# Optimization experiments

Hardware: AMD Instinct MI355X
Metric: run time of the kernel (lower is better)

## Reference

```python
import jax, jax.numpy as jnp
import numpy as np

EPSILON = 0.01            # params.epsilon (cluster precision regularizer)
GAMMA = 0.005             # params.gamma (outlier/uniform component weight)
FIX_CLUSTER_POS_ITER = 1  # params.fix_cluster_pos_iter


def _sqdist(TVs, X):
    # TVs: (M, 3, N) transformed points, X: (K, 3) cluster means -> (M, N, K)
    return ((TVs ** 2).sum(1)[:, :, None]
            + (X ** 2).sum(1)[None, None, :]
            - 2.0 * jnp.einsum('mdn,kd->mnk', TVs, X))


def setup_inputs() -> dict:
    key = jax.random.key(0)
    kV, kX, kQ = jax.random.split(key, 3)
    M, N, K = 8, 8192, 256
    Vs = jax.random.normal(kV, (M, 3, N), dtype=jnp.float32)      # 3D point clouds
    X0 = jax.random.normal(kX, (K, 3), dtype=jnp.float32)         # init cluster means (sphere init)
    Q0 = 0.1 + 0.2 * jax.random.uniform(kQ, (K,), dtype=jnp.float32)  # init cluster precisions
    return {"Vs": Vs, "X0": X0, "Q0": Q0, "num_iters": 6}


def reference(Vs, X0, Q0, num_iters):
    M, _, N = Vs.shape
    K = X0.shape[0]
    dtype = Vs.dtype

    # mean_init: init_R = I, init_t = -mean(V) per view
    t0 = -Vs.mean(axis=2, keepdims=True)          # (M, 3, 1)
    TVs = Vs + t0
    beta = GAMMA * jnp.mean(Q0) ** 1.5            # get_default_beta(Q, gamma)

    X, Q = X0, Q0
    ds = _sqdist(TVs, X)                          # (M, N, K)
    R = jnp.broadcast_to(jnp.eye(3, dtype=dtype), (M, 3, 3))
    t = t0[:, :, 0]

    for i in range(num_iters):
        if i != num_iters - 1:  # detach everything except backprop_iter = [last]
            X = jax.lax.stop_gradient(X)
            Q = jax.lax.stop_gradient(Q)
            ds = jax.lax.stop_gradient(ds)

        # E-step: soft posteriors with uniform outlier component beta
        ap = jnp.exp(-0.5 * ds * Q) * Q ** 1.5    # (M, N, K); priors = 1, pyz_feature = 1
        a = ap / (ap.sum(axis=-1, keepdims=True) + beta)

        # M-step: weighted sufficient statistics
        L = a.sum(axis=1)                                   # (M, K)
        W = jnp.einsum('mdn,mnk->mdk', Vs, a) * Q           # (M, 3, K)
        mW = W.sum(axis=-1)                                 # (M, 3)
        b = L * Q                                           # (M, K)
        mX = jnp.einsum('mk,kd->md', b, X)                  # (M, 3)
        z = b.sum(axis=-1)                                  # (M,)

        # P = (W @ X)^T - mX mW^T / z  : 3x3 weighted cross-covariance per view
        P = (jnp.einsum('mdk,ke->med', W, X)
             - mX[:, :, None] * mW[:, None, :] / z[:, None, None])

        # batched Procrustes: R = U diag(1,1,det(U V^T)) V^T
        U, _, Vt = jnp.linalg.svd(P)
        det = jnp.linalg.det(jnp.einsum('mij,mjk->mik', U, Vt))
        sgn = jnp.concatenate([jnp.ones((M, 2), dtype), det[:, None]], axis=1)
        R = jnp.einsum('mij,mjk->mik', U * sgn[:, None, :], Vt)   # (M, 3, 3)
        t = (mX - jnp.einsum('mij,mj->mi', R, mW)) / z[:, None]   # (M, 3)
        TVs = jnp.einsum('mij,mjn->min', R, Vs) + t[:, :, None]   # (M, 3, N)

        # shared cluster updates (sum over views)
        den = L.sum(axis=0)                                 # (K,)
        if i > FIX_CLUSTER_POS_ITER:
            X = jnp.einsum('mdn,mnk->kd', TVs, a) / den[:, None]
        ds = _sqdist(TVs, X)
        wn = (a * ds).sum(axis=(0, 1))                      # (K,)
        Q = 3.0 * den / (wn + 3.0 * den * EPSILON)

    return TVs, R, t, X
```

## Files before the change

kernel.cpp:

```cpp
#include <hip/hip_runtime.h>
#include <math.h>

#define Mv 8
#define Nv 8192
#define Kv 256
#define BPM 64
#define NBLK (Mv*BPM)
#define NITER 6
#define EPSILON_C 0.01f
#define GAMMA_C 0.005f

#define WS_R     0
#define WS_T     72
#define WS_X     96
#define WS_Q     864
#define WS_BETA  1120
#define WS_ACC   1124
#define AC_STATS 0
#define AC_L     128
#define AC_W     2176
#define AC_H     8320
#define ACCSZ    10368

__device__ __forceinline__ float wave_red_sum(float x) {
  int v;
  float t;
  v = __builtin_bit_cast(int, x);
  t = __builtin_bit_cast(float, __builtin_amdgcn_update_dpp(0, v, 0x111, 0xf, 0xf, true));
  x += t; v = __builtin_bit_cast(int, x);
  t = __builtin_bit_cast(float, __builtin_amdgcn_update_dpp(0, v, 0x112, 0xf, 0xf, true));
  x += t; v = __builtin_bit_cast(int, x);
  t = __builtin_bit_cast(float, __builtin_amdgcn_update_dpp(0, v, 0x114, 0xf, 0xf, true));
  x += t; v = __builtin_bit_cast(int, x);
  t = __builtin_bit_cast(float, __builtin_amdgcn_update_dpp(0, v, 0x118, 0xf, 0xf, true));
  x += t; v = __builtin_bit_cast(int, x);
  t = __builtin_bit_cast(float, __builtin_amdgcn_update_dpp(0, v, 0x142, 0xa, 0xf, false));
  x += t; v = __builtin_bit_cast(int, x);
  t = __builtin_bit_cast(float, __builtin_amdgcn_update_dpp(0, v, 0x143, 0xc, 0xf, false));
  x += t;
  return __builtin_bit_cast(float, __builtin_amdgcn_readlane(__builtin_bit_cast(int, x), 63));
}

__global__ __launch_bounds__(256) void p0_init(const float* __restrict__ Vs,
                                               const float* __restrict__ X0,
                                               const float* __restrict__ Q0,
                                               float* __restrict__ ws) {
  __shared__ float sred[4];
  int tid = threadIdx.x;
  int b = blockIdx.x;
  int wave = tid >> 6, lane = tid & 63;
  if (b < 24) {
    int m = b / 3, d = b % 3;
    const float* src = Vs + (size_t)(m*3 + d) * Nv;
    float s = 0.f;
    for (int n = tid; n < Nv; n += 256) s += src[n];
    s = wave_red_sum(s);
    if (lane == 0) sred[wave] = s;
    __syncthreads();
    if (tid == 0) {
      float tot = sred[0]+sred[1]+sred[2]+sred[3];
      ws[WS_T + m*3 + d] = -tot / (float)Nv;
    }
    if (d == 0 && tid < 9) {
      ws[WS_R + m*9 + tid] = (tid==0||tid==4||tid==8) ? 1.f : 0.f;
    }
  } else {
    float s = (tid < Kv) ? Q0[tid] : 0.f;
    s = wave_red_sum(s);
    if (lane == 0) sred[wave] = s;
    __syncthreads();
    if (tid == 0) {
      float mq = (sred[0]+sred[1]+sred[2]+sred[3]) / (float)Kv;
      ws[WS_BETA] = GAMMA_C * mq * sqrtf(mq);
    }
    if (tid < Kv) ws[WS_Q + tid] = Q0[tid];
    for (int i = tid; i < Kv*3; i += 256) ws[WS_X + i] = X0[i];
    for (int i = tid; i < ACCSZ; i += 256) ws[WS_ACC + i] = 0.f;
  }
}

#define JROTF(app,aqq,apq,apr,aqr, vp0,vp1,vp2, vq0,vq1,vq2) do {           \
    float tau_ = (aqq - app) * __builtin_amdgcn_rcpf(2.0f*apq);             \
    float tt_ = __builtin_amdgcn_rcpf(fabsf(tau_) +                         \
                   __builtin_amdgcn_sqrtf(fmaf(tau_,tau_,1.0f)));           \
    tt_ = (tau_ < 0.0f) ? -tt_ : tt_;                                       \
    tt_ = (apq == 0.0f) ? 0.0f : tt_;                                       \
    float c_ = __builtin_amdgcn_rsqf(fmaf(tt_,tt_,1.0f)), s_ = tt_*c_;      \
    float papq_ = apq;                                                      \
    app = fmaf(-tt_,papq_,app); aqq = fmaf(tt_,papq_,aqq); apq = 0.0f;      \
    float tp_ = apr, tq_ = aqr;                                             \
    apr = c_*tp_ - s_*tq_; aqr = s_*tp_ + c_*tq_;                           \
    tp_=vp0; tq_=vq0; vp0=c_*tp_-s_*tq_; vq0=s_*tp_+c_*tq_;                 \
    tp_=vp1; tq_=vq1; vp1=c_*tp_-s_*tq_; vq1=s_*tp_+c_*tq_;                 \
    tp_=vp2; tq_=vq2; vp2=c_*tp_-s_*tq_; vq2=s_*tp_+c_*tq_;                 \
  } while(0)

#define CSWAP3F(la,lb, a0,a1,a2, b0,b1,b2) do {                             \
    if (la < lb) { float t_;                                                \
      t_=la; la=lb; lb=t_; t_=a0; a0=b0; b0=t_;                             \
      t_=a1; a1=b1; b1=t_; t_=a2; a2=b2; b2=t_; }                           \
  } while(0)

template<int ITPREV>
__device__ __forceinline__ void small_update(const float* __restrict__ acc,
                                             const float* __restrict__ ws,
                                             int tid,
                                             float (*sX)[3], float* sQ,
                                             float (*sR)[9], float (*sT)[3],
                                             float* sTn) {
  const int k = tid;
  float lk[Mv], w0v[Mv], w1v[Mv], w2v[Mv], hk[Mv];
  #pragma unroll
  for (int mm=0;mm<Mv;mm++) {
    lk[mm]  = acc[AC_L + mm*Kv + k];
    w0v[mm] = acc[AC_W + (mm*3+0)*Kv + k];
    w1v[mm] = acc[AC_W + (mm*3+1)*Kv + k];
    w2v[mm] = acc[AC_W + (mm*3+2)*Kv + k];
    hk[mm]  = acc[AC_H + mm*Kv + k];
  }
  float xp0 = 0.f, xp1 = 0.f, xp2 = 0.f;
  if (ITPREV <= 1) {
    xp0 = ws[WS_X + k*3+0]; xp1 = ws[WS_X + k*3+1]; xp2 = ws[WS_X + k*3+2];
  }

  if (tid < Mv) {
    int mm = tid;
    const float* st = acc + AC_STATS + mm*16;
    float s0=st[0], s1=st[1], s2v=st[2], s3=st[3], s4=st[4], s5=st[5],
          s6=st[6], s7=st[7], s8=st[8], s9=st[9], s10=st[10], s11=st[11],
          s12=st[12], s13=st[13], s14=st[14], s15=st[15];
    float z = s0;
    float mX0 = s1, mX1 = s2v, mX2 = s3;
    float mW0 = s4, mW1 = s5, mW2 = s6;
    float iz = __builtin_amdgcn_rcpf(z);
    float P00 = s7  - mX0*mW0*iz;
    float P01 = s8  - mX0*mW1*iz;
    float P02 = s9  - mX0*mW2*iz;
    float P10 = s10 - mX1*mW0*iz;
    float P11 = s11 - mX1*mW1*iz;
    float P12 = s12 - mX1*mW2*iz;
    float P20 = s13 - mX2*mW0*iz;
    float P21 = s14 - mX2*mW1*iz;
    float P22 = s15 - mX2*mW2*iz;
    float a00 = P00*P00 + P10*P10 + P20*P20;
    float a01 = P00*P01 + P10*P11 + P20*P21;
    float a02 = P00*P02 + P10*P12 + P20*P22;
    float a11 = P01*P01 + P11*P11 + P21*P21;
    float a12 = P01*P02 + P11*P12 + P21*P22;
    float a22 = P02*P02 + P12*P12 + P22*P22;
    float v00=1, v01=0, v02=0, v10=0, v11=1, v12=0, v20=0, v21=0, v22=1;
    #pragma unroll 1
    for (int sweep = 0; sweep < 8; sweep++) {
      JROTF(a00,a11,a01, a02,a12, v00,v10,v20, v01,v11,v21);
      JROTF(a00,a22,a02, a01,a12, v00,v10,v20, v02,v12,v22);
      JROTF(a11,a22,a12, a01,a02, v01,v11,v21, v02,v12,v22);
    }
    float l0 = a00, l1 = a11, l2 = a22;
    CSWAP3F(l0,l1, v00,v10,v20, v01,v11,v21);
    CSWAP3F(l1,l2, v01,v11,v21, v02,v12,v22);
    CSWAP3F(l0,l1, v00,v10,v20, v01,v11,v21);
    float detP = P00*(P11*P22-P12*P21) - P01*(P10*P22-P12*P20)
               + P02*(P10*P21-P11*P20);
    float s2d = (detP < 0.0f) ? -1.0f : 1.0f;
    float tiny = 1e-18f*l0 + 1e-30f;
    float w0i = __builtin_amdgcn_rsqf(fmaxf(l0,tiny));
    float w1i = __builtin_amdgcn_rsqf(fmaxf(l1,tiny));
    float w2i = s2d*__builtin_amdgcn_rsqf(fmaxf(l2,tiny));
    float M00 = w0i*v00*v00 + w1i*v01*v01 + w2i*v02*v02;
    float M01 = w0i*v00*v10 + w1i*v01*v11 + w2i*v02*v12;
    float M02 = w0i*v00*v20 + w1i*v01*v21 + w2i*v02*v22;
    float M11 = w0i*v10*v10 + w1i*v11*v11 + w2i*v12*v12;
    float M12 = w0i*v10*v20 + w1i*v11*v21 + w2i*v12*v22;
    float M22 = w0i*v20*v20 + w1i*v21*v21 + w2i*v22*v22;
    float R00n = P00*M00 + P01*M01 + P02*M02;
    float R01n = P00*M01 + P01*M11 + P02*M12;
    float R02n = P00*M02 + P01*M12 + P02*M22;
    float R10n = P10*M00 + P11*M01 + P12*M02;
    float R11n = P10*M01 + P11*M11 + P12*M12;
    float R12n = P10*M02 + P11*M12 + P12*M22;
    float R20n = P20*M00 + P21*M01 + P22*M02;
    float R21n = P20*M01 + P21*M11 + P22*M12;
    float R22n = P20*M02 + P21*M12 + P22*M22;
    float tm0 = (mX0 - (R00n*mW0 + R01n*mW1 + R02n*mW2))*iz;
    float tm1 = (mX1 - (R10n*mW0 + R11n*mW1 + R12n*mW2))*iz;
    float tm2 = (mX2 - (R20n*mW0 + R21n*mW1 + R22n*mW2))*iz;
    sR[mm][0]=R00n; sR[mm][1]=R01n; sR[mm][2]=R02n;
    sR[mm][3]=R10n; sR[mm][4]=R11n; sR[mm][5]=R12n;
    sR[mm][6]=R20n; sR[mm][7]=R21n; sR[mm][8]=R22n;
    sT[mm][0]=tm0; sT[mm][1]=tm1; sT[mm][2]=tm2;
    sTn[mm] = tm0*tm0 + tm1*tm1 + tm2*tm2;
  }
  __syncthreads();
  {
    float den = 0.f, Xn0=0.f, Xn1=0.f, Xn2=0.f, S2=0.f;
    #pragma unroll
    for (int mm=0;mm<Mv;mm++) {
      float r0 = sR[mm][0]*w0v[mm] + sR[mm][1]*w1v[mm] + sR[mm][2]*w2v[mm];
      float r1 = sR[mm][3]*w0v[mm] + sR[mm][4]*w1v[mm] + sR[mm][5]*w2v[mm];
      float r2 = sR[mm][6]*w0v[mm] + sR[mm][7]*w1v[mm] + sR[mm][8]*w2v[mm];
      float tt0 = sT[mm][0], tt1 = sT[mm][1], tt2 = sT[mm][2];
      den += lk[mm];
      Xn0 += r0 + tt0*lk[mm]; Xn1 += r1 + tt1*lk[mm]; Xn2 += r2 + tt2*lk[mm];
      S2  += hk[mm] + 2.f*(tt0*r0+tt1*r1+tt2*r2) + sTn[mm]*lk[mm];
    }
    float x0, x1, x2;
    if (ITPREV > 1) { float inv = __builtin_amdgcn_rcpf(den);
                      x0=Xn0*inv; x1=Xn1*inv; x2=Xn2*inv; }
    else            { x0=xp0; x1=xp1; x2=xp2; }
    float wn = S2 + (x0*x0+x1*x1+x2*x2)*den - 2.f*(x0*Xn0+x1*Xn1+x2*Xn2);
    float qn = 3.f*den / (wn + 3.f*den*EPSILON_C);
    sX[k][0]=x0; sX[k][1]=x1; sX[k][2]=x2;
    sQ[k] = qn;
  }
}

template<int IT>
__global__ __launch_bounds__(256) void p_iter(const float* __restrict__ Vs,
                                              float* __restrict__ ws) {
  __shared__ float sb[4][5][Kv];
  __shared__ float st4[4][16];
  __shared__ float sX[Kv][3];
  __shared__ float sQ[Kv];
  __shared__ float sR[Mv][9];
  __shared__ float sT[Mv][3];
  __shared__ float sTn[Mv];

  int tid  = threadIdx.x;
  int wave = tid >> 6, lane = tid & 63;
  int bid  = blockIdx.x;
  int m    = bid / BPM;
  int blk  = bid % BPM;
  int wid  = blk*4 + wave;
  const int k = tid;

  float* acc  = ws + WS_ACC + (IT % 3)*ACCSZ;
  float* accz = ws + WS_ACC + ((IT+1) % 3)*ACCSZ;
  float beta = ws[WS_BETA];

  if (IT == 0) {
    if (tid < 72) ((float*)sR)[tid] = ws[WS_R + tid];
    if (tid < 24) ((float*)sT)[tid] = ws[WS_T + tid];
    sX[k][0] = ws[WS_X + 3*k+0];
    sX[k][1] = ws[WS_X + 3*k+1];
    sX[k][2] = ws[WS_X + 3*k+2];
    sQ[k]    = ws[WS_Q + k];
  } else {
    const float* accp = ws + WS_ACC + ((IT+2) % 3)*ACCSZ;
    small_update<(IT > 0) ? (IT-1) : 0>(accp, ws, tid, sX, sQ, sR, sT, sTn);
  }
  __syncthreads();

  { int base = bid*21;
    if (tid < 21 && base + tid < ACCSZ) accz[base + tid] = 0.f; }

  float R00=sR[m][0],R01=sR[m][1],R02=sR[m][2];
  float R10=sR[m][3],R11=sR[m][4],R12=sR[m][5];
  float R20=sR[m][6],R21=sR[m][7],R22=sR[m][8];
  float t0=sT[m][0], t1=sT[m][1], t2=sT[m][2];
  float kXx[4],kXy[4],kXz[4],kA[4],kB[4],kQ[4],kQ32[4];
  #pragma unroll
  for (int j=0;j<4;j++) {
    int kk = lane + 64*j;
    float xx = sX[kk][0], xy = sX[kk][1], xz = sX[kk][2];
    float q  = sQ[kk];
    kXx[j]=xx; kXy[j]=xy; kXz[j]=xz;
    kA[j]  = -0.5f*q;
    kB[j]  = kA[j]*(xx*xx+xy*xy+xz*xz);
    kQ[j]  = q;
    kQ32[j]= q*sqrtf(q);
  }
  float aL[4]={0,0,0,0}, aWx[4]={0,0,0,0}, aWy[4]={0,0,0,0},
        aWz[4]={0,0,0,0}, aH[4]={0,0,0,0};
  const float* V0 = Vs + (size_t)(m*3+0)*Nv;
  const float* V1 = Vs + (size_t)(m*3+1)*Nv;
  const float* V2 = Vs + (size_t)(m*3+2)*Nv;
  for (int n = wid; n < Nv; n += 256) {
    float vx = V0[n], vy = V1[n], vz = V2[n];
    float px = fmaf(R00,vx, fmaf(R01,vy, fmaf(R02,vz, t0)));
    float py = fmaf(R10,vx, fmaf(R11,vy, fmaf(R12,vz, t1)));
    float pz = fmaf(R20,vx, fmaf(R21,vy, fmaf(R22,vz, t2)));
    float tvn = fmaf(px,px, fmaf(py,py, pz*pz));
    float vn  = fmaf(vx,vx, fmaf(vy,vy, vz*vz));
    float ap[4]; float s = 0.f;
    #pragma unroll
    for (int j=0;j<4;j++) {
      float dot = fmaf(px,kXx[j], fmaf(py,kXy[j], pz*kXz[j]));
      float arg = fmaf(kQ[j], dot, fmaf(kA[j], tvn, kB[j]));
      float e = __expf(arg)*kQ32[j];
      ap[j] = e; s += e;
    }
    float S = wave_red_sum(s);
    float inv = __builtin_amdgcn_rcpf(S + beta);
    #pragma unroll
    for (int j=0;j<4;j++) {
      float a = ap[j]*inv;
      aL[j] += a;
      aWx[j] = fmaf(a,vx,aWx[j]);
      aWy[j] = fmaf(a,vy,aWy[j]);
      aWz[j] = fmaf(a,vz,aWz[j]);
      aH[j]  = fmaf(a,vn,aH[j]);
    }
  }
  #pragma unroll
  for (int j=0;j<4;j++) {
    int kk = lane + 64*j;
    sb[wave][0][kk]=aL[j];  sb[wave][1][kk]=aWx[j]; sb[wave][2][kk]=aWy[j];
    sb[wave][3][kk]=aWz[j]; sb[wave][4][kk]=aH[j];
  }
  __syncthreads();
  const int k2 = (tid + 4*blk) & (Kv-1);
  float vL  = sb[0][0][k2]+sb[1][0][k2]+sb[2][0][k2]+sb[3][0][k2];
  float vWx = sb[0][1][k2]+sb[1][1][k2]+sb[2][1][k2]+sb[3][1][k2];
  float vWy = sb[0][2][k2]+sb[1][2][k2]+sb[2][2][k2]+sb[3][2][k2];
  float vWz = sb[0][3][k2]+sb[1][3][k2]+sb[2][3][k2]+sb[3][3][k2];
  float vH  = sb[0][4][k2]+sb[1][4][k2]+sb[2][4][k2]+sb[3][4][k2];
  atomicAdd(&acc[AC_L + m*Kv + k2], vL);
  atomicAdd(&acc[AC_W + (m*3+0)*Kv + k2], vWx);
  atomicAdd(&acc[AC_W + (m*3+1)*Kv + k2], vWy);
  atomicAdd(&acc[AC_W + (m*3+2)*Kv + k2], vWz);
  atomicAdd(&acc[AC_H + m*Kv + k2], vH);
  {
    float q  = sQ[k2];
    float x0 = sX[k2][0], x1 = sX[k2][1], x2 = sX[k2][2];
    float bk = vL*q;
    float sw0 = vWx*q, sw1 = vWy*q, sw2 = vWz*q;
    float pr[16];
    pr[0]=bk;  pr[1]=bk*x0; pr[2]=bk*x1; pr[3]=bk*x2;
    pr[4]=sw0; pr[5]=sw1;   pr[6]=sw2;
    pr[7]=sw0*x0;  pr[8]=sw1*x0;  pr[9]=sw2*x0;
    pr[10]=sw0*x1; pr[11]=sw1*x1; pr[12]=sw2*x1;
    pr[13]=sw0*x2; pr[14]=sw1*x2; pr[15]=sw2*x2;
    float red[16];
    #pragma unroll
    for (int v2=0; v2<16; v2++) red[v2] = wave_red_sum(pr[v2]);
    if (lane == 0) {
      #pragma unroll
      for (int v2=0; v2<16; v2++) st4[wave][v2] = red[v2];
    }
    __syncthreads();
    if (tid < 16)
      atomicAdd(&acc[AC_STATS + m*16 + ((tid + blk) & 15)],
                st4[0][(tid+blk)&15]+st4[1][(tid+blk)&15]+
                st4[2][(tid+blk)&15]+st4[3][(tid+blk)&15]);
  }
}

#define OUT_TOTAL (Mv*3*Nv + 72 + 24 + Kv*3)
__global__ __launch_bounds__(256) void p3_final(const float* __restrict__ Vs,
                                                const float* __restrict__ ws,
                                                float* __restrict__ out) {
  __shared__ float sX[Kv][3];
  __shared__ float sQ[Kv];
  __shared__ float sR[Mv][9];
  __shared__ float sT[Mv][3];
  __shared__ float sTn[Mv];
  int tid = threadIdx.x;
  const float* acc = ws + WS_ACC + ((NITER-1) % 3)*ACCSZ;
  small_update<NITER-1>(acc, ws, tid, sX, sQ, sR, sT, sTn);
  __syncthreads();

  for (int idx = blockIdx.x*256 + tid; idx < OUT_TOTAL; idx += 256*256) {
    if (idx < Mv*3*Nv) {
      int m = idx / (3*Nv);
      int r = idx % (3*Nv);
      int d = r / Nv;
      int n = r % Nv;
      float vx = Vs[(size_t)(m*3+0)*Nv + n];
      float vy = Vs[(size_t)(m*3+1)*Nv + n];
      float vz = Vs[(size_t)(m*3+2)*Nv + n];
      out[idx] = fmaf(sR[m][d*3+0],vx,
                 fmaf(sR[m][d*3+1],vy,
                 fmaf(sR[m][d*3+2],vz, sT[m][d])));
    } else {
      int j = idx - Mv*3*Nv;
      float v;
      if (j < 72)      v = ((float*)sR)[j];
      else if (j < 96) v = ((float*)sT)[j-72];
      else             v = ((float*)sX)[j-96];
      out[idx] = v;
    }
  }
}

extern "C" void kernel_launch(void* const* d_in, const int* in_sizes, int n_in,
                              void* d_out, int out_size, void* d_ws, size_t ws_size,
                              hipStream_t stream) {
  const float* Vs = (const float*)d_in[0];
  const float* X0 = (const float*)d_in[1];
  const float* Q0 = (const float*)d_in[2];
  float* out = (float*)d_out;
  float* ws  = (float*)d_ws;

  p0_init<<<25, 256, 0, stream>>>(Vs, X0, Q0, ws);
  p_iter<0><<<NBLK, 256, 0, stream>>>(Vs, ws);
  p_iter<1><<<NBLK, 256, 0, stream>>>(Vs, ws);
  p_iter<2><<<NBLK, 256, 0, stream>>>(Vs, ws);
  p_iter<3><<<NBLK, 256, 0, stream>>>(Vs, ws);
  p_iter<4><<<NBLK, 256, 0, stream>>>(Vs, ws);
  p_iter<5><<<NBLK, 256, 0, stream>>>(Vs, ws);
  p3_final<<<256, 256, 0, stream>>>(Vs, ws, out);
}
```

Measured before the change: 213.2 us.

## Run per-iteration small update once in last-arriving block instead of every block

Before, every one of the 512 blocks redundantly recomputed the cluster/rotation update (small_update, including the Jacobi SVD) at the start of each iteration. Now a ticket counter picks the last block to finish accumulation, and that block alone computes the 16 per-view statistics from the accumulated per-cluster sums and then the Procrustes and cluster update. It writes R, t, X and Q to global workspace for the next launch to read. This removes redundant per-block work and the per-block stats atomics, at the cost of a serial tail in one block per iteration. The accumulators switch to double buffering, and the final kernel reads from global memory with more blocks.

```diff
diff --git a/kernel.cpp b/kernel.cpp
--- a/kernel.cpp
+++ b/kernel.cpp
@@ -12,15 +12,15 @@
 
 #define WS_R     0
 #define WS_T     72
-#define WS_X     96
-#define WS_Q     864
+#define WS_XC    96
+#define WS_QC    864
 #define WS_BETA  1120
-#define WS_ACC   1124
-#define AC_STATS 0
-#define AC_L     128
-#define AC_W     2176
-#define AC_H     8320
-#define ACCSZ    10368
+#define WS_TKT   1124
+#define WS_ACC   1132
+#define AC_L     0
+#define AC_W     2048
+#define AC_H     8192
+#define ACCSZ    10240
 
 __device__ __forceinline__ float wave_red_sum(float x) {
   int v;
@@ -64,7 +64,7 @@
     if (d == 0 && tid < 9) {
       ws[WS_R + m*9 + tid] = (tid==0||tid==4||tid==8) ? 1.f : 0.f;
     }
-  } else {
+  } else if (b == 24) {
     float s = (tid < Kv) ? Q0[tid] : 0.f;
     s = wave_red_sum(s);
     if (lane == 0) sred[wave] = s;
@@ -73,9 +73,11 @@
       float mq = (sred[0]+sred[1]+sred[2]+sred[3]) / (float)Kv;
       ws[WS_BETA] = GAMMA_C * mq * sqrtf(mq);
     }
-    if (tid < Kv) ws[WS_Q + tid] = Q0[tid];
-    for (int i = tid; i < Kv*3; i += 256) ws[WS_X + i] = X0[i];
-    for (int i = tid; i < ACCSZ; i += 256) ws[WS_ACC + i] = 0.f;
+    if (tid < Kv) ws[WS_QC + tid] = Q0[tid];
+    for (int i = tid; i < Kv*3; i += 256) ws[WS_XC + i] = X0[i];
+  } else {
+    for (int i = tid + (b-25)*256; i < 8 + ACCSZ; i += 256*8)
+      ws[WS_TKT + i] = 0.f;
   }
 }
 
@@ -101,13 +103,110 @@
       t_=a1; a1=b1; b1=t_; t_=a2; a2=b2; b2=t_; }                           \
   } while(0)
 
-template<int ITPREV>
-__device__ __forceinline__ void small_update(const float* __restrict__ acc,
-                                             const float* __restrict__ ws,
-                                             int tid,
-                                             float (*sX)[3], float* sQ,
-                                             float (*sR)[9], float (*sT)[3],
-                                             float* sTn) {
+template<int IT>
+__global__ __launch_bounds__(256) void p_iter(const float* __restrict__ Vs,
+                                              float* __restrict__ ws) {
+  __shared__ float sb[4][5][Kv];
+  __shared__ float st4[4][128];
+  __shared__ float sStats[Mv][16];
+  __shared__ float sR[Mv][9];
+  __shared__ float sT[Mv][3];
+  __shared__ float sTn[Mv];
+  __shared__ int   sLast;
+
+  int tid  = threadIdx.x;
+  int wave = tid >> 6, lane = tid & 63;
+  int bid  = blockIdx.x;
+  int m    = bid / BPM;
+  int blk  = bid % BPM;
+  int wid  = blk*4 + wave;
+
+  float* acc  = ws + WS_ACC + (IT & 1)*ACCSZ;
+  float* accz = ws + WS_ACC + ((IT+1) & 1)*ACCSZ;
+  float beta = ws[WS_BETA];
+
+  if (tid < 20) accz[bid*20 + tid] = 0.f;
+
+  float R00=ws[WS_R+m*9+0], R01=ws[WS_R+m*9+1], R02=ws[WS_R+m*9+2];
+  float R10=ws[WS_R+m*9+3], R11=ws[WS_R+m*9+4], R12=ws[WS_R+m*9+5];
+  float R20=ws[WS_R+m*9+6], R21=ws[WS_R+m*9+7], R22=ws[WS_R+m*9+8];
+  float t0=ws[WS_T+m*3+0], t1=ws[WS_T+m*3+1], t2=ws[WS_T+m*3+2];
+  float kXx[4],kXy[4],kXz[4],kA[4],kB[4],kQ[4],kQ32[4];
+  #pragma unroll
+  for (int j=0;j<4;j++) {
+    int kk = lane + 64*j;
+    float xx = ws[WS_XC+kk*3+0], xy = ws[WS_XC+kk*3+1], xz = ws[WS_XC+kk*3+2];
+    float q  = ws[WS_QC+kk];
+    kXx[j]=xx; kXy[j]=xy; kXz[j]=xz;
+    kA[j]  = -0.5f*q;
+    kB[j]  = kA[j]*(xx*xx+xy*xy+xz*xz);
+    kQ[j]  = q;
+    kQ32[j]= q*sqrtf(q);
+  }
+
+  float aL[4]={0,0,0,0}, aWx[4]={0,0,0,0}, aWy[4]={0,0,0,0},
+        aWz[4]={0,0,0,0}, aH[4]={0,0,0,0};
+  const float* V0 = Vs + (size_t)(m*3+0)*Nv;
+  const float* V1 = Vs + (size_t)(m*3+1)*Nv;
+  const float* V2 = Vs + (size_t)(m*3+2)*Nv;
+  for (int n = wid; n < Nv; n += 256) {
+    float vx = V0[n], vy = V1[n], vz = V2[n];
+    float px = fmaf(R00,vx, fmaf(R01,vy, fmaf(R02,vz, t0)));
+    float py = fmaf(R10,vx, fmaf(R11,vy, fmaf(R12,vz, t1)));
+    float pz = fmaf(R20,vx, fmaf(R21,vy, fmaf(R22,vz, t2)));
+    float tvn = fmaf(px,px, fmaf(py,py, pz*pz));
+    float vn  = fmaf(vx,vx, fmaf(vy,vy, vz*vz));
+    float ap[4]; float s = 0.f;
+    #pragma unroll
+    for (int j=0;j<4;j++) {
+      float dot = fmaf(px,kXx[j], fmaf(py,kXy[j], pz*kXz[j]));
+      float arg = fmaf(kQ[j], dot, fmaf(kA[j], tvn, kB[j]));
+      float e = __expf(arg)*kQ32[j];
+      ap[j] = e; s += e;
+    }
+    float S = wave_red_sum(s);
+    float inv = __builtin_amdgcn_rcpf(S + beta);
+    #pragma unroll
+    for (int j=0;j<4;j++) {
+      float a = ap[j]*inv;
+      aL[j] += a;
+      aWx[j] = fmaf(a,vx,aWx[j]);
+      aWy[j] = fmaf(a,vy,aWy[j]);
+      aWz[j] = fmaf(a,vz,aWz[j]);
+      aH[j]  = fmaf(a,vn,aH[j]);
+    }
+  }
+  #pragma unroll
+  for (int j=0;j<4;j++) {
+    int kk = lane + 64*j;
+    sb[wave][0][kk]=aL[j];  sb[wave][1][kk]=aWx[j]; sb[wave][2][kk]=aWy[j];
+    sb[wave][3][kk]=aWz[j]; sb[wave][4][kk]=aH[j];
+  }
+  __syncthreads();
+  {
+    const int k2 = (tid + 4*blk) & (Kv-1);
+    float vL  = sb[0][0][k2]+sb[1][0][k2]+sb[2][0][k2]+sb[3][0][k2];
+    float vWx = sb[0][1][k2]+sb[1][1][k2]+sb[2][1][k2]+sb[3][1][k2];
+    float vWy = sb[0][2][k2]+sb[1][2][k2]+sb[2][2][k2]+sb[3][2][k2];
+    float vWz = sb[0][3][k2]+sb[1][3][k2]+sb[2][3][k2]+sb[3][3][k2];
+    float vH  = sb[0][4][k2]+sb[1][4][k2]+sb[2][4][k2]+sb[3][4][k2];
+    atomicAdd(&acc[AC_L + m*Kv + k2], vL);
+    atomicAdd(&acc[AC_W + (m*3+0)*Kv + k2], vWx);
+    atomicAdd(&acc[AC_W + (m*3+1)*Kv + k2], vWy);
+    atomicAdd(&acc[AC_W + (m*3+2)*Kv + k2], vWz);
+    atomicAdd(&acc[AC_H + m*Kv + k2], vH);
+  }
+
+  __threadfence();
+  __syncthreads();
+  if (tid == 0) {
+    unsigned old = atomicAdd((unsigned*)(ws + WS_TKT) + IT, 1u);
+    sLast = (old == (unsigned)(NBLK - 1));
+  }
+  __syncthreads();
+  if (!sLast) return;
+  __threadfence();
+
   const int k = tid;
   float lk[Mv], w0v[Mv], w1v[Mv], w2v[Mv], hk[Mv];
   #pragma unroll
@@ -118,17 +217,36 @@
     w2v[mm] = acc[AC_W + (mm*3+2)*Kv + k];
     hk[mm]  = acc[AC_H + mm*Kv + k];
   }
-  float xp0 = 0.f, xp1 = 0.f, xp2 = 0.f;
-  if (ITPREV <= 1) {
-    xp0 = ws[WS_X + k*3+0]; xp1 = ws[WS_X + k*3+1]; xp2 = ws[WS_X + k*3+2];
-  }
+  float qk  = ws[WS_QC + k];
+  float xc0 = ws[WS_XC + k*3+0], xc1 = ws[WS_XC + k*3+1], xc2 = ws[WS_XC + k*3+2];
+
+  #pragma unroll
+  for (int mm=0;mm<Mv;mm++) {
+    float bk  = lk[mm]*qk;
+    float sw0 = w0v[mm]*qk, sw1 = w1v[mm]*qk, sw2 = w2v[mm]*qk;
+    float pr[16];
+    pr[0]=bk;  pr[1]=bk*xc0; pr[2]=bk*xc1; pr[3]=bk*xc2;
+    pr[4]=sw0; pr[5]=sw1;    pr[6]=sw2;
+    pr[7]=sw0*xc0;  pr[8]=sw1*xc0;  pr[9]=sw2*xc0;
+    pr[10]=sw0*xc1; pr[11]=sw1*xc1; pr[12]=sw2*xc1;
+    pr[13]=sw0*xc2; pr[14]=sw1*xc2; pr[15]=sw2*xc2;
+    #pragma unroll
+    for (int v2=0; v2<16; v2++) {
+      float r = wave_red_sum(pr[v2]);
+      if (lane == 0) st4[wave][mm*16+v2] = r;
+    }
+  }
+  __syncthreads();
+  if (tid < 128)
+    sStats[tid>>4][tid&15] = st4[0][tid]+st4[1][tid]+st4[2][tid]+st4[3][tid];
+  __syncthreads();
 
   if (tid < Mv) {
     int mm = tid;
-    const float* st = acc + AC_STATS + mm*16;
-    float s0=st[0], s1=st[1], s2v=st[2], s3=st[3], s4=st[4], s5=st[5],
-          s6=st[6], s7=st[7], s8=st[8], s9=st[9], s10=st[10], s11=st[11],
-          s12=st[12], s13=st[13], s14=st[14], s15=st[15];
+    float s0=sStats[mm][0], s1=sStats[mm][1], s2v=sStats[mm][2], s3=sStats[mm][3],
+          s4=sStats[mm][4], s5=sStats[mm][5], s6=sStats[mm][6], s7=sStats[mm][7],
+          s8=sStats[mm][8], s9=sStats[mm][9], s10=sStats[mm][10], s11=sStats[mm][11],
+          s12=sStats[mm][12], s13=sStats[mm][13], s14=sStats[mm][14], s15=sStats[mm][15];
     float z = s0;
     float mX0 = s1, mX1 = s2v, mX2 = s3;
     float mW0 = s4, mW1 = s5, mW2 = s6;
@@ -204,162 +322,23 @@
       S2  += hk[mm] + 2.f*(tt0*r0+tt1*r1+tt2*r2) + sTn[mm]*lk[mm];
     }
     float x0, x1, x2;
-    if (ITPREV > 1) { float inv = __builtin_amdgcn_rcpf(den);
-                      x0=Xn0*inv; x1=Xn1*inv; x2=Xn2*inv; }
-    else            { x0=xp0; x1=xp1; x2=xp2; }
+    if (IT > 1) { float inv = __builtin_amdgcn_rcpf(den);
+                  x0=Xn0*inv; x1=Xn1*inv; x2=Xn2*inv; }
+    else        { x0=xc0; x1=xc1; x2=xc2; }
     float wn = S2 + (x0*x0+x1*x1+x2*x2)*den - 2.f*(x0*Xn0+x1*Xn1+x2*Xn2);
     float qn = 3.f*den / (wn + 3.f*den*EPSILON_C);
-    sX[k][0]=x0; sX[k][1]=x1; sX[k][2]=x2;
-    sQ[k] = qn;
-  }
-}
-
-template<int IT>
-__global__ __launch_bounds__(256) void p_iter(const float* __restrict__ Vs,
-                                              float* __restrict__ ws) {
-  __shared__ float sb[4][5][Kv];
-  __shared__ float st4[4][16];
-  __shared__ float sX[Kv][3];
-  __shared__ float sQ[Kv];
-  __shared__ float sR[Mv][9];
-  __shared__ float sT[Mv][3];
-  __shared__ float sTn[Mv];
-
-  int tid  = threadIdx.x;
-  int wave = tid >> 6, lane = tid & 63;
-  int bid  = blockIdx.x;
-  int m    = bid / BPM;
-  int blk  = bid % BPM;
-  int wid  = blk*4 + wave;
-  const int k = tid;
-
-  float* acc  = ws + WS_ACC + (IT % 3)*ACCSZ;
-  float* accz = ws + WS_ACC + ((IT+1) % 3)*ACCSZ;
-  float beta = ws[WS_BETA];
-
-  if (IT == 0) {
-    if (tid < 72) ((float*)sR)[tid] = ws[WS_R + tid];
-    if (tid < 24) ((float*)sT)[tid] = ws[WS_T + tid];
-    sX[k][0] = ws[WS_X + 3*k+0];
-    sX[k][1] = ws[WS_X + 3*k+1];
-    sX[k][2] = ws[WS_X + 3*k+2];
-    sQ[k]    = ws[WS_Q + k];
-  } else {
-    const float* accp = ws + WS_ACC + ((IT+2) % 3)*ACCSZ;
-    small_update<(IT > 0) ? (IT-1) : 0>(accp, ws, tid, sX, sQ, sR, sT, sTn);
-  }
-  __syncthreads();
-
-  { int base = bid*21;
-    if (tid < 21 && base + tid < ACCSZ) accz[base + tid] = 0.f; }
-
-  float R00=sR[m][0],R01=sR[m][1],R02=sR[m][2];
-  float R10=sR[m][3],R11=sR[m][4],R12=sR[m][5];
-  float R20=sR[m][6],R21=sR[m][7],R22=sR[m][8];
-  float t0=sT[m][0], t1=sT[m][1], t2=sT[m][2];
-  float kXx[4],kXy[4],kXz[4],kA[4],kB[4],kQ[4],kQ32[4];
-  #pragma unroll
-  for (int j=0;j<4;j++) {
-    int kk = lane + 64*j;
-    float xx = sX[kk][0], xy = sX[kk][1], xz = sX[kk][2];
-    float q  = sQ[kk];
-    kXx[j]=xx; kXy[j]=xy; kXz[j]=xz;
-    kA[j]  = -0.5f*q;
-    kB[j]  = kA[j]*(xx*xx+xy*xy+xz*xz);
-    kQ[j]  = q;
-    kQ32[j]= q*sqrtf(q);
-  }
-  float aL[4]={0,0,0,0}, aWx[4]={0,0,0,0}, aWy[4]={0,0,0,0},
-        aWz[4]={0,0,0,0}, aH[4]={0,0,0,0};
-  const float* V0 = Vs + (size_t)(m*3+0)*Nv;
-  const float* V1 = Vs + (size_t)(m*3+1)*Nv;
-  const float* V2 = Vs + (size_t)(m*3+2)*Nv;
-  for (int n = wid; n < Nv; n += 256) {
-    float vx = V0[n], vy = V1[n], vz = V2[n];
-    float px = fmaf(R00,vx, fmaf(R01,vy, fmaf(R02,vz, t0)));
-    float py = fmaf(R10,vx, fmaf(R11,vy, fmaf(R12,vz, t1)));
-    float pz = fmaf(R20,vx, fmaf(R21,vy, fmaf(R22,vz, t2)));
-    float tvn = fmaf(px,px, fmaf(py,py, pz*pz));
-    float vn  = fmaf(vx,vx, fmaf(vy,vy, vz*vz));
-    float ap[4]; float s = 0.f;
-    #pragma unroll
-    for (int j=0;j<4;j++) {
-      float dot = fmaf(px,kXx[j], fmaf(py,kXy[j], pz*kXz[j]));
-      float arg = fmaf(kQ[j], dot, fmaf(kA[j], tvn, kB[j]));
-      float e = __expf(arg)*kQ32[j];
-      ap[j] = e; s += e;
-    }
-    float S = wave_red_sum(s);
-    float inv = __builtin_amdgcn_rcpf(S + beta);
-    #pragma unroll
-    for (int j=0;j<4;j++) {
-      float a = ap[j]*inv;
-      aL[j] += a;
-      aWx[j] = fmaf(a,vx,aWx[j]);
-      aWy[j] = fmaf(a,vy,aWy[j]);
-      aWz[j] = fmaf(a,vz,aWz[j]);
-      aH[j]  = fmaf(a,vn,aH[j]);
-    }
-  }
-  #pragma unroll
-  for (int j=0;j<4;j++) {
-    int kk = lane + 64*j;
-    sb[wave][0][kk]=aL[j];  sb[wave][1][kk]=aWx[j]; sb[wave][2][kk]=aWy[j];
-    sb[wave][3][kk]=aWz[j]; sb[wave][4][kk]=aH[j];
-  }
-  __syncthreads();
-  const int k2 = (tid + 4*blk) & (Kv-1);
-  float vL  = sb[0][0][k2]+sb[1][0][k2]+sb[2][0][k2]+sb[3][0][k2];
-  float vWx = sb[0][1][k2]+sb[1][1][k2]+sb[2][1][k2]+sb[3][1][k2];
-  float vWy = sb[0][2][k2]+sb[1][2][k2]+sb[2][2][k2]+sb[3][2][k2];
-  float vWz = sb[0][3][k2]+sb[1][3][k2]+sb[2][3][k2]+sb[3][3][k2];
-  float vH  = sb[0][4][k2]+sb[1][4][k2]+sb[2][4][k2]+sb[3][4][k2];
-  atomicAdd(&acc[AC_L + m*Kv + k2], vL);
-  atomicAdd(&acc[AC_W + (m*3+0)*Kv + k2], vWx);
-  atomicAdd(&acc[AC_W + (m*3+1)*Kv + k2], vWy);
-  atomicAdd(&acc[AC_W + (m*3+2)*Kv + k2], vWz);
-  atomicAdd(&acc[AC_H + m*Kv + k2], vH);
-  {
-    float q  = sQ[k2];
-    float x0 = sX[k2][0], x1 = sX[k2][1], x2 = sX[k2][2];
-    float bk = vL*q;
-    float sw0 = vWx*q, sw1 = vWy*q, sw2 = vWz*q;
-    float pr[16];
-    pr[0]=bk;  pr[1]=bk*x0; pr[2]=bk*x1; pr[3]=bk*x2;
-    pr[4]=sw0; pr[5]=sw1;   pr[6]=sw2;
-    pr[7]=sw0*x0;  pr[8]=sw1*x0;  pr[9]=sw2*x0;
-    pr[10]=sw0*x1; pr[11]=sw1*x1; pr[12]=sw2*x1;
-    pr[13]=sw0*x2; pr[14]=sw1*x2; pr[15]=sw2*x2;
-    float red[16];
-    #pragma unroll
-    for (int v2=0; v2<16; v2++) red[v2] = wave_red_sum(pr[v2]);
-    if (lane == 0) {
-      #pragma unroll
-      for (int v2=0; v2<16; v2++) st4[wave][v2] = red[v2];
-    }
-    __syncthreads();
-    if (tid < 16)
-      atomicAdd(&acc[AC_STATS + m*16 + ((tid + blk) & 15)],
-                st4[0][(tid+blk)&15]+st4[1][(tid+blk)&15]+
-                st4[2][(tid+blk)&15]+st4[3][(tid+blk)&15]);
-  }
+    ws[WS_XC + k*3+0]=x0; ws[WS_XC + k*3+1]=x1; ws[WS_XC + k*3+2]=x2;
+    ws[WS_QC + k] = qn;
+  }
+  if (tid < 72) ws[WS_R + tid] = ((float*)sR)[tid];
+  if (tid < 24) ws[WS_T + tid] = ((float*)sT)[tid];
 }
 
 #define OUT_TOTAL (Mv*3*Nv + 72 + 24 + Kv*3)
 __global__ __launch_bounds__(256) void p3_final(const float* __restrict__ Vs,
                                                 const float* __restrict__ ws,
                                                 float* __restrict__ out) {
-  __shared__ float sX[Kv][3];
-  __shared__ float sQ[Kv];
-  __shared__ float sR[Mv][9];
-  __shared__ float sT[Mv][3];
-  __shared__ float sTn[Mv];
-  int tid = threadIdx.x;
-  const float* acc = ws + WS_ACC + ((NITER-1) % 3)*ACCSZ;
-  small_update<NITER-1>(acc, ws, tid, sX, sQ, sR, sT, sTn);
-  __syncthreads();
-
-  for (int idx = blockIdx.x*256 + tid; idx < OUT_TOTAL; idx += 256*256) {
+  for (int idx = blockIdx.x*256 + threadIdx.x; idx < OUT_TOTAL; idx += 512*256) {
     if (idx < Mv*3*Nv) {
       int m = idx / (3*Nv);
       int r = idx % (3*Nv);
@@ -368,15 +347,15 @@
       float vx = Vs[(size_t)(m*3+0)*Nv + n];
       float vy = Vs[(size_t)(m*3+1)*Nv + n];
       float vz = Vs[(size_t)(m*3+2)*Nv + n];
-      out[idx] = fmaf(sR[m][d*3+0],vx,
-                 fmaf(sR[m][d*3+1],vy,
-                 fmaf(sR[m][d*3+2],vz, sT[m][d])));
+      out[idx] = fmaf(ws[WS_R+m*9+d*3+0],vx,
+                 fmaf(ws[WS_R+m*9+d*3+1],vy,
+                 fmaf(ws[WS_R+m*9+d*3+2],vz, ws[WS_T+m*3+d])));
     } else {
       int j = idx - Mv*3*Nv;
       float v;
-      if (j < 72)      v = ((float*)sR)[j];
-      else if (j < 96) v = ((float*)sT)[j-72];
-      else             v = ((float*)sX)[j-96];
+      if (j < 72)      v = ws[WS_R + j];
+      else if (j < 96) v = ws[WS_T + (j-72)];
+      else             v = ws[WS_XC + (j-96)];
       out[idx] = v;
     }
   }
@@ -391,12 +370,12 @@
   float* out = (float*)d_out;
   float* ws  = (float*)d_ws;
 
-  p0_init<<<25, 256, 0, stream>>>(Vs, X0, Q0, ws);
+  p0_init<<<33, 256, 0, stream>>>(Vs, X0, Q0, ws);
   p_iter<0><<<NBLK, 256, 0, stream>>>(Vs, ws);
   p_iter<1><<<NBLK, 256, 0, stream>>>(Vs, ws);
   p_iter<2><<<NBLK, 256, 0, stream>>>(Vs, ws);
   p_iter<3><<<NBLK, 256, 0, stream>>>(Vs, ws);
   p_iter<4><<<NBLK, 256, 0, stream>>>(Vs, ws);
   p_iter<5><<<NBLK, 256, 0, stream>>>(Vs, ws);
-  p3_final<<<256, 256, 0, stream>>>(Vs, ws, out);
-}
+  p3_final<<<512, 256, 0, stream>>>(Vs, ws, out);
+}
```

Result: slower. 419.0 us (+96.6%).

## Replace atomic accumulation with per-block partials and a separate reduce kernel

Applied to the files above, without the earlier changes.

Each iteration kernel now writes per-block partial sums (L, W, H) to a workspace slab instead of issuing global atomicAdds. A new small kernel with one block per view sums the 64 partials and computes the 16 Procrustes statistics. Cluster X/Q are ping-ponged in workspace instead of the triple-buffered accumulators, and the final kernel launches 512 blocks. This removes atomic contention and accumulator zeroing, at the cost of six extra kernel launches, each running only 8 blocks.

```diff
diff --git a/kernel.cpp b/kernel.cpp
--- a/kernel.cpp
+++ b/kernel.cpp
@@ -12,15 +12,12 @@
 
 #define WS_R     0
 #define WS_T     72
-#define WS_X     96
-#define WS_Q     864
-#define WS_BETA  1120
-#define WS_ACC   1124
-#define AC_STATS 0
-#define AC_L     128
-#define AC_W     2176
-#define AC_H     8320
-#define ACCSZ    10368
+#define WS_XC    96
+#define WS_QC    1632
+#define WS_BETA  2144
+#define WS_TOT   2148
+#define WS_STATS 12388
+#define WS_PART  12516
 
 __device__ __forceinline__ float wave_red_sum(float x) {
   int v;
@@ -73,9 +70,8 @@
       float mq = (sred[0]+sred[1]+sred[2]+sred[3]) / (float)Kv;
       ws[WS_BETA] = GAMMA_C * mq * sqrtf(mq);
     }
-    if (tid < Kv) ws[WS_Q + tid] = Q0[tid];
-    for (int i = tid; i < Kv*3; i += 256) ws[WS_X + i] = X0[i];
-    for (int i = tid; i < ACCSZ; i += 256) ws[WS_ACC + i] = 0.f;
+    if (tid < Kv) ws[WS_QC + tid] = Q0[tid];
+    for (int i = tid; i < Kv*3; i += 256) ws[WS_XC + i] = X0[i];
   }
 }
 
@@ -102,30 +98,28 @@
   } while(0)
 
 template<int ITPREV>
-__device__ __forceinline__ void small_update(const float* __restrict__ acc,
-                                             const float* __restrict__ ws,
-                                             int tid,
-                                             float (*sX)[3], float* sQ,
-                                             float (*sR)[9], float (*sT)[3],
-                                             float* sTn) {
+__device__ __forceinline__ void small_update2(const float* __restrict__ ws,
+                                              int tid,
+                                              float (*sX)[3], float* sQ,
+                                              float (*sR)[9], float (*sT)[3],
+                                              float* sTn) {
   const int k = tid;
   float lk[Mv], w0v[Mv], w1v[Mv], w2v[Mv], hk[Mv];
   #pragma unroll
   for (int mm=0;mm<Mv;mm++) {
-    lk[mm]  = acc[AC_L + mm*Kv + k];
-    w0v[mm] = acc[AC_W + (mm*3+0)*Kv + k];
-    w1v[mm] = acc[AC_W + (mm*3+1)*Kv + k];
-    w2v[mm] = acc[AC_W + (mm*3+2)*Kv + k];
-    hk[mm]  = acc[AC_H + mm*Kv + k];
-  }
-  float xp0 = 0.f, xp1 = 0.f, xp2 = 0.f;
-  if (ITPREV <= 1) {
-    xp0 = ws[WS_X + k*3+0]; xp1 = ws[WS_X + k*3+1]; xp2 = ws[WS_X + k*3+2];
-  }
+    const float* t5 = ws + WS_TOT + (mm*5)*Kv + k;
+    lk[mm]  = t5[0*Kv];
+    w0v[mm] = t5[1*Kv];
+    w1v[mm] = t5[2*Kv];
+    w2v[mm] = t5[3*Kv];
+    hk[mm]  = t5[4*Kv];
+  }
+  const float* xcp = ws + WS_XC + (ITPREV&1)*768;
+  float xp0 = xcp[k*3+0], xp1 = xcp[k*3+1], xp2 = xcp[k*3+2];
 
   if (tid < Mv) {
     int mm = tid;
-    const float* st = acc + AC_STATS + mm*16;
+    const float* st = ws + WS_STATS + mm*16;
     float s0=st[0], s1=st[1], s2v=st[2], s3=st[3], s4=st[4], s5=st[5],
           s6=st[6], s7=st[7], s8=st[8], s9=st[9], s10=st[10], s11=st[11],
           s12=st[12], s13=st[13], s14=st[14], s15=st[15];
@@ -215,10 +209,9 @@
 }
 
 template<int IT>
-__global__ __launch_bounds__(256) void p_iter(const float* __restrict__ Vs,
-                                              float* __restrict__ ws) {
+__global__ __launch_bounds__(256) void pA(const float* __restrict__ Vs,
+                                          float* __restrict__ ws) {
   __shared__ float sb[4][5][Kv];
-  __shared__ float st4[4][16];
   __shared__ float sX[Kv][3];
   __shared__ float sQ[Kv];
   __shared__ float sR[Mv][9];
@@ -232,26 +225,24 @@
   int blk  = bid % BPM;
   int wid  = blk*4 + wave;
   const int k = tid;
-
-  float* acc  = ws + WS_ACC + (IT % 3)*ACCSZ;
-  float* accz = ws + WS_ACC + ((IT+1) % 3)*ACCSZ;
   float beta = ws[WS_BETA];
 
   if (IT == 0) {
     if (tid < 72) ((float*)sR)[tid] = ws[WS_R + tid];
     if (tid < 24) ((float*)sT)[tid] = ws[WS_T + tid];
-    sX[k][0] = ws[WS_X + 3*k+0];
-    sX[k][1] = ws[WS_X + 3*k+1];
-    sX[k][2] = ws[WS_X + 3*k+2];
-    sQ[k]    = ws[WS_Q + k];
+    sX[k][0] = ws[WS_XC + 3*k+0];
+    sX[k][1] = ws[WS_XC + 3*k+1];
+    sX[k][2] = ws[WS_XC + 3*k+2];
+    sQ[k]    = ws[WS_QC + k];
   } else {
-    const float* accp = ws + WS_ACC + ((IT+2) % 3)*ACCSZ;
-    small_update<(IT > 0) ? (IT-1) : 0>(accp, ws, tid, sX, sQ, sR, sT, sTn);
+    small_update2<(IT > 0) ? (IT-1) : 0>(ws, tid, sX, sQ, sR, sT, sTn);
   }
   __syncthreads();
-
-  { int base = bid*21;
-    if (tid < 21 && base + tid < ACCSZ) accz[base + tid] = 0.f; }
+  if (IT > 0 && bid == 0) {
+    float* xcn = ws + WS_XC + (IT&1)*768;
+    xcn[k*3+0]=sX[k][0]; xcn[k*3+1]=sX[k][1]; xcn[k*3+2]=sX[k][2];
+    ws[WS_QC + (IT&1)*Kv + k] = sQ[k];
+  }
 
   float R00=sR[m][0],R01=sR[m][1],R02=sR[m][2];
   float R10=sR[m][3],R11=sR[m][4],R12=sR[m][5];
@@ -308,41 +299,55 @@
     sb[wave][3][kk]=aWz[j]; sb[wave][4][kk]=aH[j];
   }
   __syncthreads();
-  const int k2 = (tid + 4*blk) & (Kv-1);
-  float vL  = sb[0][0][k2]+sb[1][0][k2]+sb[2][0][k2]+sb[3][0][k2];
-  float vWx = sb[0][1][k2]+sb[1][1][k2]+sb[2][1][k2]+sb[3][1][k2];
-  float vWy = sb[0][2][k2]+sb[1][2][k2]+sb[2][2][k2]+sb[3][2][k2];
-  float vWz = sb[0][3][k2]+sb[1][3][k2]+sb[2][3][k2]+sb[3][3][k2];
-  float vH  = sb[0][4][k2]+sb[1][4][k2]+sb[2][4][k2]+sb[3][4][k2];
-  atomicAdd(&acc[AC_L + m*Kv + k2], vL);
-  atomicAdd(&acc[AC_W + (m*3+0)*Kv + k2], vWx);
-  atomicAdd(&acc[AC_W + (m*3+1)*Kv + k2], vWy);
-  atomicAdd(&acc[AC_W + (m*3+2)*Kv + k2], vWz);
-  atomicAdd(&acc[AC_H + m*Kv + k2], vH);
-  {
-    float q  = sQ[k2];
-    float x0 = sX[k2][0], x1 = sX[k2][1], x2 = sX[k2][2];
-    float bk = vL*q;
-    float sw0 = vWx*q, sw1 = vWy*q, sw2 = vWz*q;
-    float pr[16];
-    pr[0]=bk;  pr[1]=bk*x0; pr[2]=bk*x1; pr[3]=bk*x2;
-    pr[4]=sw0; pr[5]=sw1;   pr[6]=sw2;
-    pr[7]=sw0*x0;  pr[8]=sw1*x0;  pr[9]=sw2*x0;
-    pr[10]=sw0*x1; pr[11]=sw1*x1; pr[12]=sw2*x1;
-    pr[13]=sw0*x2; pr[14]=sw1*x2; pr[15]=sw2*x2;
-    float red[16];
+  float* pb = ws + WS_PART + (size_t)((m*BPM + blk)*5)*Kv;
+  pb[0*Kv + k] = sb[0][0][k]+sb[1][0][k]+sb[2][0][k]+sb[3][0][k];
+  pb[1*Kv + k] = sb[0][1][k]+sb[1][1][k]+sb[2][1][k]+sb[3][1][k];
+  pb[2*Kv + k] = sb[0][2][k]+sb[1][2][k]+sb[2][2][k]+sb[3][2][k];
+  pb[3*Kv + k] = sb[0][3][k]+sb[1][3][k]+sb[2][3][k]+sb[3][3][k];
+  pb[4*Kv + k] = sb[0][4][k]+sb[1][4][k]+sb[2][4][k]+sb[3][4][k];
+}
+
+__global__ __launch_bounds__(256) void pB1(float* __restrict__ ws, int par) {
+  __shared__ float st4[4][16];
+  int tid = threadIdx.x;
+  int wave = tid >> 6, lane = tid & 63;
+  int m = blockIdx.x;
+  float tL=0.f, tWx=0.f, tWy=0.f, tWz=0.f, tH=0.f;
+  const float* P = ws + WS_PART + (size_t)(m*BPM*5)*Kv;
+  #pragma unroll 4
+  for (int blk = 0; blk < BPM; ++blk) {
+    const float* b = P + blk*5*Kv;
+    tL  += b[0*Kv + tid];
+    tWx += b[1*Kv + tid];
+    tWy += b[2*Kv + tid];
+    tWz += b[3*Kv + tid];
+    tH  += b[4*Kv + tid];
+  }
+  float* t5 = ws + WS_TOT + (m*5)*Kv + tid;
+  t5[0*Kv]=tL; t5[1*Kv]=tWx; t5[2*Kv]=tWy; t5[3*Kv]=tWz; t5[4*Kv]=tH;
+
+  float q  = ws[WS_QC + par*Kv + tid];
+  const float* xc = ws + WS_XC + par*768;
+  float x0 = xc[tid*3+0], x1 = xc[tid*3+1], x2 = xc[tid*3+2];
+  float bk = tL*q;
+  float sw0 = tWx*q, sw1 = tWy*q, sw2 = tWz*q;
+  float pr[16];
+  pr[0]=bk;  pr[1]=bk*x0; pr[2]=bk*x1; pr[3]=bk*x2;
+  pr[4]=sw0; pr[5]=sw1;   pr[6]=sw2;
+  pr[7]=sw0*x0;  pr[8]=sw1*x0;  pr[9]=sw2*x0;
+  pr[10]=sw0*x1; pr[11]=sw1*x1; pr[12]=sw2*x1;
+  pr[13]=sw0*x2; pr[14]=sw1*x2; pr[15]=sw2*x2;
+  float red[16];
+  #pragma unroll
+  for (int v2=0; v2<16; v2++) red[v2] = wave_red_sum(pr[v2]);
+  if (lane == 0) {
     #pragma unroll
-    for (int v2=0; v2<16; v2++) red[v2] = wave_red_sum(pr[v2]);
-    if (lane == 0) {
-      #pragma unroll
-      for (int v2=0; v2<16; v2++) st4[wave][v2] = red[v2];
-    }
-    __syncthreads();
-    if (tid < 16)
-      atomicAdd(&acc[AC_STATS + m*16 + ((tid + blk) & 15)],
-                st4[0][(tid+blk)&15]+st4[1][(tid+blk)&15]+
-                st4[2][(tid+blk)&15]+st4[3][(tid+blk)&15]);
-  }
+    for (int v2=0; v2<16; v2++) st4[wave][v2] = red[v2];
+  }
+  __syncthreads();
+  if (tid < 16)
+    ws[WS_STATS + m*16 + tid] =
+        st4[0][tid]+st4[1][tid]+st4[2][tid]+st4[3][tid];
 }
 
 #define OUT_TOTAL (Mv*3*Nv + 72 + 24 + Kv*3)
@@ -355,11 +360,10 @@
   __shared__ float sT[Mv][3];
   __shared__ float sTn[Mv];
   int tid = threadIdx.x;
-  const float* acc = ws + WS_ACC + ((NITER-1) % 3)*ACCSZ;
-  small_update<NITER-1>(acc, ws, tid, sX, sQ, sR, sT, sTn);
+  small_update2<NITER-1>(ws, tid, sX, sQ, sR, sT, sTn);
   __syncthreads();
 
-  for (int idx = blockIdx.x*256 + tid; idx < OUT_TOTAL; idx += 256*256) {
+  for (int idx = blockIdx.x*256 + tid; idx < OUT_TOTAL; idx += 512*256) {
     if (idx < Mv*3*Nv) {
       int m = idx / (3*Nv);
       int r = idx % (3*Nv);
@@ -392,11 +396,17 @@
   float* ws  = (float*)d_ws;
 
   p0_init<<<25, 256, 0, stream>>>(Vs, X0, Q0, ws);
-  p_iter<0><<<NBLK, 256, 0, stream>>>(Vs, ws);
-  p_iter<1><<<NBLK, 256, 0, stream>>>(Vs, ws);
-  p_iter<2><<<NBLK, 256, 0, stream>>>(Vs, ws);
-  p_iter<3><<<NBLK, 256, 0, stream>>>(Vs, ws);
-  p_iter<4><<<NBLK, 256, 0, stream>>>(Vs, ws);
-  p_iter<5><<<NBLK, 256, 0, stream>>>(Vs, ws);
-  p3_final<<<256, 256, 0, stream>>>(Vs, ws, out);
-}
+  pA<0><<<NBLK, 256, 0, stream>>>(Vs, ws);
+  pB1<<<Mv, 256, 0, stream>>>(ws, 0);
+  pA<1><<<NBLK, 256, 0, stream>>>(Vs, ws);
+  pB1<<<Mv, 256, 0, stream>>>(ws, 1);
+  pA<2><<<NBLK, 256, 0, stream>>>(Vs, ws);
+  pB1<<<Mv, 256, 0, stream>>>(ws, 0);
+  pA<3><<<NBLK, 256, 0, stream>>>(Vs, ws);
+  pB1<<<Mv, 256, 0, stream>>>(ws, 1);
+  pA<4><<<NBLK, 256, 0, stream>>>(Vs, ws);
+  pB1<<<Mv, 256, 0, stream>>>(ws, 0);
+  pA<5><<<NBLK, 256, 0, stream>>>(Vs, ws);
+  pB1<<<Mv, 256, 0, stream>>>(ws, 1);
+  p3_final<<<512, 256, 0, stream>>>(Vs, ws, out);
+}
```

Measured after the change: 253.2 us. +18.8%, slower.
